# Optimization experiments

Measured on AMD Instinct MI355X. Metric: run time of the kernel, lower is better.

The kernel has to match this reference:

```python
import jax, jax.numpy as jnp
import numpy as np

NUM_USERS = 100000
NUM_MOVIES = 50000
NUM_EDGES = 4000000
USER_FEAT = 24
MOVIE_FEAT = 404
HID = 64
GENRES = 3


def setup_inputs() -> dict:
    key = jax.random.key(0)
    ks = jax.random.split(key, 16)
    inp = {
        'x_user': jax.random.normal(ks[0], (NUM_USERS, USER_FEAT), jnp.float32),
        'x_movie': jax.random.normal(ks[1], (NUM_MOVIES, MOVIE_FEAT), jnp.float32),
        'edge_src': jax.random.randint(ks[2], (NUM_EDGES,), 0, NUM_USERS, jnp.int32),
        'edge_dst': jax.random.randint(ks[3], (NUM_EDGES,), 0, NUM_MOVIES, jnp.int32),
        'W_user': jax.random.normal(ks[4], (HID, USER_FEAT), jnp.float32) * 0.1,
        'b_user': jax.random.normal(ks[5], (HID,), jnp.float32) * 0.1,
        'W_movie': jax.random.normal(ks[6], (HID, MOVIE_FEAT), jnp.float32) * 0.05,
        'b_movie': jax.random.normal(ks[7], (HID,), jnp.float32) * 0.1,
        'Wl1_um': jax.random.normal(ks[8], (HID, HID), jnp.float32) * 0.1,
        'bl1_um': jax.random.normal(ks[9], (HID,), jnp.float32) * 0.1,
        'Wr1_um': jax.random.normal(ks[10], (HID, HID), jnp.float32) * 0.1,
        'Wl1_mu': jax.random.normal(ks[11], (HID, HID), jnp.float32) * 0.1,
        'bl1_mu': jax.random.normal(ks[12], (HID,), jnp.float32) * 0.1,
        'Wr1_mu': jax.random.normal(ks[13], (HID, HID), jnp.float32) * 0.1,
        'Wl2_um': jax.random.normal(ks[14], (GENRES, HID), jnp.float32) * 0.1,
        'bl2_um': jnp.zeros((GENRES,), jnp.float32),
        'Wr2_um': jax.random.normal(ks[15], (GENRES, HID), jnp.float32) * 0.1,
    }
    return inp


def _mean_agg(src_x, src_idx, dst_idx, num_dst):
    # gather messages [E, C], scatter-sum to dst, divide by degree (mean aggr)
    msg = src_x[src_idx]
    s = jax.ops.segment_sum(msg, dst_idx, num_segments=num_dst)
    cnt = jax.ops.segment_sum(jnp.ones_like(dst_idx, jnp.float32), dst_idx, num_segments=num_dst)
    return s / jnp.maximum(cnt, 1.0)[:, None]


def _sage(agg, x_dst, Wl, bl, Wr):
    # SAGEConv: lin_l(mean_aggr(x_j)) + lin_r(x_dst); bias only on lin_l
    return agg @ Wl.T + bl + x_dst @ Wr.T


def reference(x_user, x_movie, edge_src, edge_dst, W_user, b_user, W_movie, b_movie,
              Wl1_um, bl1_um, Wr1_um, Wl1_mu, bl1_mu, Wr1_mu, Wl2_um, bl2_um, Wr2_um):
    nu, nm = x_user.shape[0], x_movie.shape[0]
    # input projections
    hu = x_user @ W_user.T + b_user    # [U, H]
    hm = x_movie @ W_movie.T + b_movie  # [M, H]
    # layer 1 (hetero: one SAGEConv per edge type; undirected -> both directions)
    m1 = _sage(_mean_agg(hu, edge_src, edge_dst, nm), hm, Wl1_um, bl1_um, Wr1_um)
    u1 = _sage(_mean_agg(hm, edge_dst, edge_src, nu), hu, Wl1_mu, bl1_mu, Wr1_mu)
    m1 = jax.nn.relu(m1)
    u1 = jax.nn.relu(u1)
    # dropout is identity in eval mode
    # layer 2: only movie output is returned
    out = _sage(_mean_agg(u1, edge_src, edge_dst, nm), m1, Wl2_um, bl2_um, Wr2_um)
    return out
```

## Files before the change

kernel.cpp:

```cpp
#include <hip/hip_runtime.h>


constexpr int NU = 100000;
constexpr int NM = 50000;
constexpr int NE = 4000000;
constexpr int FU = 24;
constexpr int FM = 404;
constexpr int HD = 64;

constexpr int BSH = 8;
constexpr int MBK = (NM + 255) >> BSH;
constexpr int UBK = (NU + 255) >> BSH;
constexpr int NBK = MBK + UBK;
constexpr int EPB = 8192;
constexpr int CAPE = 28672;

static inline size_t alignup(size_t x) { return (x + 255) & ~size_t(255); }

__device__ __forceinline__ float bf2f(unsigned short h) {
  return __uint_as_float(((unsigned int)h) << 16);
}
__device__ __forceinline__ unsigned short f2bf(float f) {
  unsigned int u = __float_as_uint(f);
  u = (u + 0x7FFFu + ((u >> 16) & 1u)) >> 16;
  return (unsigned short)u;
}
__device__ __forceinline__ float2 unpk(unsigned u) {
  return make_float2(__uint_as_float(u << 16), __uint_as_float(u & 0xFFFF0000u));
}
__device__ __forceinline__ float fp8dec(unsigned v) {
  unsigned u = ((v & 0x80u) << 24) | ((v & 0x7Fu) << 20);
  return __uint_as_float(u) * 0x1p120f;
}
__device__ __forceinline__ unsigned char f2fp8(float f) {
  float a = fminf(fabsf(f), 448.0f);
  unsigned u = __float_as_uint(a * 0x1p-120f);
  u = u + 0x7FFFFu + ((u >> 20) & 1u);
  return (unsigned char)(((u >> 20) & 0x7Fu) | ((__float_as_uint(f) >> 24) & 0x80u));
}

typedef __attribute__((ext_vector_type(2))) float f2v;

#if __has_builtin(__builtin_amdgcn_cvt_pk_f32_fp8)
#define FP8_HW 1
#endif

__device__ __forceinline__ f2v fp8lo(unsigned w) {
#ifdef FP8_HW
  return __builtin_amdgcn_cvt_pk_f32_fp8(w, false);
#else
  f2v r; r.x = fp8dec(w); r.y = fp8dec(w >> 8); return r;
#endif
}
__device__ __forceinline__ f2v fp8hi(unsigned w) {
#ifdef FP8_HW
  return __builtin_amdgcn_cvt_pk_f32_fp8(w, true);
#else
  f2v r; r.x = fp8dec(w >> 16); r.y = fp8dec(w >> 24); return r;
#endif
}

using bf16x8 = __attribute__((ext_vector_type(8))) short;
using f32x4  = __attribute__((ext_vector_type(4))) float;


__global__ __launch_bounds__(256) void histB_kernel(const int* __restrict__ src,
                                                    const int* __restrict__ dst,
                                                    int* __restrict__ bh) {
  __shared__ int h[NBK];
  for (int i = threadIdx.x; i < NBK; i += 256) h[i] = 0;
  __syncthreads();
  int idx = blockIdx.x * 256 + threadIdx.x;
  int stride = gridDim.x * 256;
  for (int i = idx; i < NE; i += stride) {
    atomicAdd(&h[dst[i] >> BSH], 1);
    atomicAdd(&h[MBK + (src[i] >> BSH)], 1);
  }
  __syncthreads();
  for (int i = threadIdx.x; i < NBK; i += 256) {
    int c = h[i];
    if (c) atomicAdd(&bh[i], c);
  }
}

__global__ __launch_bounds__(1024) void scanB_kernel(const int* __restrict__ bh,
                                                     int* __restrict__ bbase_m,
                                                     int* __restrict__ bbase_u,
                                                     int* __restrict__ bcur_m,
                                                     int* __restrict__ bcur_u) {
  __shared__ int tmp[1024];
  int t = threadIdx.x;
  int vm = (t < MBK) ? bh[t] : 0;
  tmp[t] = vm;
  __syncthreads();
  for (int off = 1; off < 1024; off <<= 1) {
    int v = (t >= off) ? tmp[t - off] : 0;
    __syncthreads();
    tmp[t] += v;
    __syncthreads();
  }
  if (t < MBK) {
    int e = tmp[t] - vm;
    bbase_m[t] = e; bcur_m[t] = e;
    if (t == MBK - 1) bbase_m[MBK] = tmp[t];
  }
  __syncthreads();
  int vu = (t < UBK) ? bh[MBK + t] : 0;
  tmp[t] = vu;
  __syncthreads();
  for (int off = 1; off < 1024; off <<= 1) {
    int v = (t >= off) ? tmp[t - off] : 0;
    __syncthreads();
    tmp[t] += v;
    __syncthreads();
  }
  if (t < UBK) {
    int e = tmp[t] - vu;
    bbase_u[t] = e; bcur_u[t] = e;
    if (t == UBK - 1) bbase_u[UBK] = tmp[t];
  }
}

__global__ __launch_bounds__(1024) void passA_kernel(
    const int* __restrict__ src, const int* __restrict__ dst,
    int* __restrict__ bcur_m, int* __restrict__ bcur_u,
    unsigned* __restrict__ stage_m, unsigned* __restrict__ stage_u) {
  __shared__ int hB[NBK];
  __shared__ int cntB[NBK];
  __shared__ int gB[NBK];
  __shared__ int tmp[1024];
  __shared__ unsigned binM[EPB];
  __shared__ unsigned binU[EPB];
  int t = threadIdx.x;
  for (int i = t; i < NBK; i += 1024) hB[i] = 0;
  __syncthreads();
  int e0 = blockIdx.x * EPB + t;
  int sv[8], dv[8], rm[8], ru[8];
#pragma unroll
  for (int k = 0; k < 8; ++k) {
    int e = e0 + k * 1024;
    if (e < NE) {
      int s = src[e], d = dst[e];
      sv[k] = s; dv[k] = d;
      rm[k] = atomicAdd(&hB[d >> BSH], 1);
      ru[k] = atomicAdd(&hB[MBK + (s >> BSH)], 1);
    } else {
      sv[k] = -1;
    }
  }
  __syncthreads();
  int cm = (t < MBK) ? hB[t] : 0;
  tmp[t] = cm;
  __syncthreads();
  for (int off = 1; off < 1024; off <<= 1) {
    int v = (t >= off) ? tmp[t - off] : 0;
    __syncthreads();
    tmp[t] += v;
    __syncthreads();
  }
  int lofsM = tmp[t] - cm;
  __syncthreads();
  int cu_ = (t < UBK) ? hB[MBK + t] : 0;
  tmp[t] = cu_;
  __syncthreads();
  for (int off = 1; off < 1024; off <<= 1) {
    int v = (t >= off) ? tmp[t - off] : 0;
    __syncthreads();
    tmp[t] += v;
    __syncthreads();
  }
  int lofsU = tmp[t] - cu_;
  __syncthreads();
  if (t < MBK) { cntB[t] = cm; hB[t] = lofsM; }
  if (t < UBK) { cntB[MBK + t] = cu_; hB[MBK + t] = lofsU; }
  __syncthreads();
#pragma unroll
  for (int k = 0; k < 8; ++k) {
    if (sv[k] >= 0) {
      int s = sv[k], d = dv[k];
      binM[hB[d >> BSH] + rm[k]] = ((unsigned)(d & 255) << 24) | (unsigned)s;
      binU[hB[MBK + (s >> BSH)] + ru[k]] = ((unsigned)(s & 255) << 24) | (unsigned)d;
    }
  }
  __syncthreads();
  for (int b = t; b < NBK; b += 1024) {
    int cc = cntB[b];
    if (cc) {
      int gb = (b < MBK) ? atomicAdd(&bcur_m[b], cc) : atomicAdd(&bcur_u[b - MBK], cc);
      gB[b] = gb - hB[b];
    }
  }
  __syncthreads();
  int wv = t >> 6, ln = t & 63;
  for (int b = wv; b < MBK; b += 16) {
    int cc = cntB[b], lo = hB[b], go = hB[b] + gB[b];
    for (int j = ln; j < cc; j += 64) stage_m[go + j] = binM[lo + j];
  }
  for (int b = wv; b < UBK; b += 16) {
    int cc = cntB[MBK + b], lo = hB[MBK + b], go = hB[MBK + b] + gB[MBK + b];
    for (int j = ln; j < cc; j += 64) stage_u[go + j] = binU[lo + j];
  }
}

__global__ __launch_bounds__(1024) void passB_kernel(
    const int* __restrict__ bbase_m, const int* __restrict__ bbase_u,
    const unsigned* __restrict__ stage_m, const unsigned* __restrict__ stage_u,
    int* __restrict__ csr_m, int* __restrict__ csr_u,
    int* __restrict__ rp_m, int* __restrict__ rp_u) {
  __shared__ int cnt[256];
  __shared__ int sc[256];
  extern __shared__ unsigned sbuf[];
  int b = blockIdx.x;
  const unsigned* stage; int* csr; int* rp; int idbase, ntot, bb, be;
  if (b < MBK) {
    stage = stage_m; csr = csr_m; rp = rp_m;
    idbase = b << BSH; ntot = NM;
    bb = bbase_m[b]; be = bbase_m[b + 1];
  } else {
    int c = b - MBK;
    stage = stage_u; csr = csr_u; rp = rp_u;
    idbase = c << BSH; ntot = NU;
    bb = bbase_u[c]; be = bbase_u[c + 1];
  }
  int nloc = min(256, ntot - idbase);
  int t = threadIdx.x;
  int span = be - bb;
  if (t < 256) cnt[t] = 0;
  __syncthreads();
  for (int j = bb + t; j < be; j += 1024) atomicAdd(&cnt[stage[j] >> 24], 1);
  __syncthreads();
  int c0 = (t < 256) ? cnt[t] : 0;
  if (t < 256) sc[t] = c0;
  __syncthreads();
  for (int off = 1; off < 256; off <<= 1) {
    int v = 0;
    if (t < 256 && t >= off) v = sc[t - off];
    __syncthreads();
    if (t < 256) sc[t] += v;
    __syncthreads();
  }
  if (t < nloc) {
    rp[idbase + t] = bb + sc[t] - c0;
    cnt[t] = sc[t] - c0;
  }
  if (t == 0 && idbase + nloc == ntot) rp[ntot] = be;
  __syncthreads();
  if (span <= CAPE) {
    for (int j = bb + t; j < be; j += 1024) {
      unsigned e = stage[j];
      int pos = atomicAdd(&cnt[e >> 24], 1);
      sbuf[pos] = e & 0xFFFFFFu;
    }
    __syncthreads();
    for (int j = t; j < span; j += 1024) csr[bb + j] = (int)sbuf[j];
  } else {
    for (int j = bb + t; j < be; j += 1024) {
      unsigned e = stage[j];
      int pos = atomicAdd(&cnt[e >> 24], 1);
      csr[bb + pos] = (int)(e & 0xFFFFFFu);
    }
  }
}


__global__ void convXu_kernel(const float* __restrict__ xu, unsigned char* __restrict__ xu8) {
  int i = blockIdx.x * 256 + threadIdx.x;
  if (i < NU * 32) {
    int r = i >> 5, c = i & 31;
    xu8[i] = (c < FU) ? f2fp8(xu[r * FU + c]) : 0;
  }
}

__global__ void convXu16_kernel(const float* __restrict__ xu, unsigned short* __restrict__ xb) {
  int i = blockIdx.x * 256 + threadIdx.x;
  if (i < NU * 32) {
    int r = i >> 5, c = i & 31;
    unsigned short v = 0;
    if (c < FU) v = f2bf(xu[r * FU + c]);
    else if (c == 31) v = 0x3F80;
    xb[i] = v;
  }
}

__global__ void convW_kernel(const float* __restrict__ W, unsigned short* __restrict__ Wb,
                             int n) {
  int i = blockIdx.x * 256 + threadIdx.x;
  if (i < n) Wb[i] = f2bf(W[i]);
}

__global__ void convWum_kernel(const float* __restrict__ Wl, const float* __restrict__ Wu,
                               const float* __restrict__ bu, const float* __restrict__ Wr,
                               unsigned short* __restrict__ W96) {
  int i = blockIdx.x * 256 + threadIdx.x;
  if (i >= 64 * 96) return;
  int h = i / 96, k = i - h * 96;
  float v = 0.f;
  if (k < FU) {
    for (int j = 0; j < 64; ++j) v += Wl[h * 64 + j] * Wu[j * FU + k];
  } else if (k == 31) {
    for (int j = 0; j < 64; ++j) v += Wl[h * 64 + j] * bu[j];
  } else if (k >= 32) {
    v = Wr[h * 64 + (k - 32)];
  }
  W96[i] = f2bf(v);
}

__global__ void convWmu_kernel(const float* __restrict__ Wl, const float* __restrict__ Wr,
                               const float* __restrict__ Wu, const float* __restrict__ bu,
                               unsigned short* __restrict__ W96) {
  int i = blockIdx.x * 256 + threadIdx.x;
  if (i >= 64 * 96) return;
  int h = i / 96, k = i - h * 96;
  float v = 0.f;
  if (k < 64) {
    v = Wl[h * 64 + k];
  } else if (k < 64 + FU) {
    for (int j = 0; j < 64; ++j) v += Wr[h * 64 + j] * Wu[j * FU + (k - 64)];
  } else if (k == 95) {
    for (int j = 0; j < 64; ++j) v += Wr[h * 64 + j] * bu[j];
  }
  W96[i] = f2bf(v);
}

__global__ __launch_bounds__(256) void proj_movie_kernel(
    const float* __restrict__ xm, const unsigned short* __restrict__ Wb,
    const float* __restrict__ bm, unsigned short* __restrict__ hm,
    unsigned char* __restrict__ hm8) {
  __shared__ unsigned short Xs[64][72];
  __shared__ unsigned short Ws[64][72];
  int t = threadIdx.x;
  int lane = t & 63, wid = t >> 6;
  int row0 = blockIdx.x * 64;
  int r0 = wid * 16;
  f32x4 acc[4];
#pragma unroll
  for (int nt = 0; nt < 4; ++nt) acc[nt] = (f32x4){0.f, 0.f, 0.f, 0.f};

  for (int k0 = 0; k0 < 448; k0 += 64) {
    int kc = min(64, FM - k0);
    __syncthreads();
    for (int i = t; i < 1024; i += 256) {
      int r = i >> 4, c4 = i & 15;
      float4 v = make_float4(0.f, 0.f, 0.f, 0.f);
      if (c4 * 4 < kc && row0 + r < NM)
        v = *(const float4*)(xm + (size_t)(row0 + r) * FM + k0 + c4 * 4);
      ushort4 o;
      o.x = f2bf(v.x); o.y = f2bf(v.y); o.z = f2bf(v.z); o.w = f2bf(v.w);
      *(ushort4*)&Xs[r][c4 * 4] = o;
    }
    for (int i = t; i < 1024; i += 256) {
      int h = i >> 4, c4 = i & 15;
      uint2 v = make_uint2(0u, 0u);
      if (c4 * 4 < kc)
        v = *(const uint2*)(Wb + (size_t)h * FM + k0 + c4 * 4);
      *(uint2*)&Ws[h][c4 * 4] = v;
    }
    __syncthreads();
#pragma unroll
    for (int kk = 0; kk < 64; kk += 32) {
      bf16x8 a = *(const bf16x8*)&Xs[r0 + (lane & 15)][kk + (lane >> 4) * 8];
#pragma unroll
      for (int nt = 0; nt < 4; ++nt) {
        bf16x8 b = *(const bf16x8*)&Ws[nt * 16 + (lane & 15)][kk + (lane >> 4) * 8];
        acc[nt] = __builtin_amdgcn_mfma_f32_16x16x32_bf16(a, b, acc[nt], 0, 0, 0);
      }
    }
  }
  int col = lane & 15;
  int rbase = r0 + (lane >> 4) * 4;
#pragma unroll
  for (int nt = 0; nt < 4; ++nt) {
    float b = bm[nt * 16 + col];
#pragma unroll
    for (int j = 0; j < 4; ++j) {
      int row = row0 + rbase + j;
      if (row < NM) {
        float v = acc[nt][j] + b;
        hm[(size_t)row * HD + nt * 16 + col] = f2bf(v);
        hm8[(size_t)row * HD + nt * 16 + col] = f2fp8(v);
      }
    }
  }
}


__global__ __launch_bounds__(256) void agg24z_kernel(
    const unsigned char* __restrict__ xu8, const int* __restrict__ rp,
    const int* __restrict__ csr, unsigned short* __restrict__ a24,
    float* __restrict__ zagg, int n) {
  int wid = threadIdx.x >> 6, lane = threadIdx.x & 63;
  int row = blockIdx.x * 4 + wid;
  if (row >= n) return;
  int beg = rp[row], end = rp[row + 1];
  int g = lane >> 2;
  int fq = lane & 3;
  const unsigned char* tb = xu8 + fq * 8;
  f2v a01 = {0.f, 0.f}, a23 = {0.f, 0.f}, a45 = {0.f, 0.f}, a67 = {0.f, 0.f};
  int i = beg;
  for (; i + 32 <= end; i += 32) {
    unsigned o0 = (unsigned)csr[i + g] << 5;
    unsigned o1 = (unsigned)csr[i + 16 + g] << 5;
    uint2 w0 = *(const uint2*)(tb + o0);
    uint2 w1 = *(const uint2*)(tb + o1);
    a01 += fp8lo(w0.x) + fp8lo(w1.x);
    a23 += fp8hi(w0.x) + fp8hi(w1.x);
    a45 += fp8lo(w0.y) + fp8lo(w1.y);
    a67 += fp8hi(w0.y) + fp8hi(w1.y);
  }
  for (; i < end; i += 16) {
    int idx = i + g;
    if (idx < end) {
      unsigned o = (unsigned)csr[idx] << 5;
      uint2 w = *(const uint2*)(tb + o);
      a01 += fp8lo(w.x); a23 += fp8hi(w.x);
      a45 += fp8lo(w.y); a67 += fp8hi(w.y);
    }
  }
  float a[8] = {a01.x, a01.y, a23.x, a23.y, a45.x, a45.y, a67.x, a67.y};
#pragma unroll
  for (int off = 4; off < 64; off <<= 1)
#pragma unroll
    for (int j = 0; j < 8; ++j) a[j] += __shfl_xor(a[j], off);
  if (g == 0) {
    float inv = 1.0f / fmaxf((float)(end - beg), 1.0f);
    uint4 o;
    o.x = (unsigned)f2bf(a[0] * inv) | ((unsigned)f2bf(a[1] * inv) << 16);
    o.y = (unsigned)f2bf(a[2] * inv) | ((unsigned)f2bf(a[3] * inv) << 16);
    o.z = (unsigned)f2bf(a[4] * inv) | ((unsigned)f2bf(a[5] * inv) << 16);
    o.w = (unsigned)f2bf(a[6] * inv) | ((unsigned)f2bf(a[7] * inv) << 16);
    if (fq == 3) {
      o.w = (o.w & 0xFFFFu) | ((end > beg ? 0x3F80u : 0u) << 16);
      *(float4*)(zagg + (size_t)row * 4) =
          make_float4(a[0] * inv, a[1] * inv, a[2] * inv, 0.f);
    }
    *(uint4*)(a24 + (size_t)row * 32 + fq * 8) = o;
  }
}


__global__ __launch_bounds__(256) void aggU_kernel(
    const unsigned char* __restrict__ tab8, const int* __restrict__ rp,
    const int* __restrict__ csr, unsigned short* __restrict__ out, int n) {
  int wid = threadIdx.x >> 6, lane = threadIdx.x & 63;
  int row = blockIdx.x * 4 + wid;
  if (row >= n) return;
  int beg = rp[row], end = rp[row + 1];
  int g = lane >> 3;
  int fq = lane & 7;
  const unsigned char* tb = tab8 + fq * 8;
  f2v a01 = {0.f, 0.f}, a23 = {0.f, 0.f}, a45 = {0.f, 0.f}, a67 = {0.f, 0.f};
  int i = beg;
  for (; i + 32 <= end; i += 32) {
    unsigned o0 = (unsigned)csr[i + g] << 6;
    unsigned o1 = (unsigned)csr[i + 8 + g] << 6;
    unsigned o2 = (unsigned)csr[i + 16 + g] << 6;
    unsigned o3 = (unsigned)csr[i + 24 + g] << 6;
    uint2 w0 = *(const uint2*)(tb + o0);
    uint2 w1 = *(const uint2*)(tb + o1);
    uint2 w2 = *(const uint2*)(tb + o2);
    uint2 w3 = *(const uint2*)(tb + o3);
    a01 += (fp8lo(w0.x) + fp8lo(w1.x)) + (fp8lo(w2.x) + fp8lo(w3.x));
    a23 += (fp8hi(w0.x) + fp8hi(w1.x)) + (fp8hi(w2.x) + fp8hi(w3.x));
    a45 += (fp8lo(w0.y) + fp8lo(w1.y)) + (fp8lo(w2.y) + fp8lo(w3.y));
    a67 += (fp8hi(w0.y) + fp8hi(w1.y)) + (fp8hi(w2.y) + fp8hi(w3.y));
  }
  for (; i + 16 <= end; i += 16) {
    unsigned o0 = (unsigned)csr[i + g] << 6;
    unsigned o1 = (unsigned)csr[i + 8 + g] << 6;
    uint2 w0 = *(const uint2*)(tb + o0);
    uint2 w1 = *(const uint2*)(tb + o1);
    a01 += fp8lo(w0.x) + fp8lo(w1.x);
    a23 += fp8hi(w0.x) + fp8hi(w1.x);
    a45 += fp8lo(w0.y) + fp8lo(w1.y);
    a67 += fp8hi(w0.y) + fp8hi(w1.y);
  }
  for (; i < end; i += 8) {
    int idx = i + g;
    if (idx < end) {
      unsigned o = (unsigned)csr[idx] << 6;
      uint2 w = *(const uint2*)(tb + o);
      a01 += fp8lo(w.x); a23 += fp8hi(w.x);
      a45 += fp8lo(w.y); a67 += fp8hi(w.y);
    }
  }
  float a[8] = {a01.x, a01.y, a23.x, a23.y, a45.x, a45.y, a67.x, a67.y};
#pragma unroll
  for (int off = 8; off < 64; off <<= 1)
#pragma unroll
    for (int j = 0; j < 8; ++j) a[j] += __shfl_xor(a[j], off);
  if (g == 0) {
    float inv = 1.0f / fmaxf((float)(end - beg), 1.0f);
    uint4 o;
    o.x = (unsigned)f2bf(a[0] * inv) | ((unsigned)f2bf(a[1] * inv) << 16);
    o.y = (unsigned)f2bf(a[2] * inv) | ((unsigned)f2bf(a[3] * inv) << 16);
    o.z = (unsigned)f2bf(a[4] * inv) | ((unsigned)f2bf(a[5] * inv) << 16);
    o.w = (unsigned)f2bf(a[6] * inv) | ((unsigned)f2bf(a[7] * inv) << 16);
    *(uint4*)(out + (size_t)row * HD + fq * 8) = o;
  }
}


__global__ __launch_bounds__(256) void sage_um_kernel(
    const unsigned short* __restrict__ a24, const unsigned short* __restrict__ hm,
    const unsigned short* __restrict__ W96, const float* __restrict__ bl,
    unsigned short* __restrict__ m1, int n) {
  __shared__ unsigned short Xs[64][104];
  __shared__ unsigned short Ws[64][104];
  int t = threadIdx.x;
  int lane = t & 63, wid = t >> 6;
  int row0 = blockIdx.x * 64;
  int r0 = wid * 16;
  for (int i = t; i < 768; i += 256) {
    int h = i / 12, g = i - h * 12;
    *(uint4*)&Ws[h][g * 8] = *(const uint4*)(W96 + (size_t)h * 96 + g * 8);
  }
  for (int i = t; i < 768; i += 256) {
    int r = i / 12, g = i - r * 12;
    uint4 v = make_uint4(0u, 0u, 0u, 0u);
    if (row0 + r < n) {
      if (g < 4) v = *(const uint4*)(a24 + (size_t)(row0 + r) * 32 + g * 8);
      else       v = *(const uint4*)(hm + (size_t)(row0 + r) * HD + (g - 4) * 8);
    }
    *(uint4*)&Xs[r][g * 8] = v;
  }
  __syncthreads();
  f32x4 acc[4];
#pragma unroll
  for (int nt = 0; nt < 4; ++nt) acc[nt] = (f32x4){0.f, 0.f, 0.f, 0.f};
#pragma unroll
  for (int kk = 0; kk < 96; kk += 32) {
    bf16x8 a = *(const bf16x8*)&Xs[r0 + (lane & 15)][kk + (lane >> 4) * 8];
#pragma unroll
    for (int nt = 0; nt < 4; ++nt) {
      bf16x8 b = *(const bf16x8*)&Ws[nt * 16 + (lane & 15)][kk + (lane >> 4) * 8];
      acc[nt] = __builtin_amdgcn_mfma_f32_16x16x32_bf16(a, b, acc[nt], 0, 0, 0);
    }
  }
  int col = lane & 15;
  int rbase = r0 + (lane >> 4) * 4;
#pragma unroll
  for (int nt = 0; nt < 4; ++nt) {
    float b = bl[nt * 16 + col];
#pragma unroll
    for (int j = 0; j < 4; ++j) {
      int row = row0 + rbase + j;
      if (row < n)
        m1[(size_t)row * HD + nt * 16 + col] = f2bf(fmaxf(acc[nt][j] + b, 0.f));
    }
  }
}


__global__ __launch_bounds__(256) void sage96u_kernel(
    const unsigned short* __restrict__ agg, const unsigned short* __restrict__ xb,
    const unsigned short* __restrict__ W96, const float* __restrict__ bl,
    unsigned short* __restrict__ u1, int n) {
  __shared__ unsigned short Xs[64][104];
  __shared__ unsigned short Ws[64][104];
  int t = threadIdx.x;
  int lane = t & 63, wid = t >> 6;
  int row0 = blockIdx.x * 64;
  int r0 = wid * 16;
  for (int i = t; i < 768; i += 256) {
    int h = i / 12, g = i - h * 12;
    *(uint4*)&Ws[h][g * 8] = *(const uint4*)(W96 + (size_t)h * 96 + g * 8);
  }
  for (int i = t; i < 768; i += 256) {
    int r = i / 12, g = i - r * 12;
    uint4 v = make_uint4(0u, 0u, 0u, 0u);
    if (row0 + r < n) {
      if (g < 8) v = *(const uint4*)(agg + (size_t)(row0 + r) * HD + g * 8);
      else       v = *(const uint4*)(xb + (size_t)(row0 + r) * 32 + (g - 8) * 8);
    }
    *(uint4*)&Xs[r][g * 8] = v;
  }
  __syncthreads();
  f32x4 acc[4];
#pragma unroll
  for (int nt = 0; nt < 4; ++nt) acc[nt] = (f32x4){0.f, 0.f, 0.f, 0.f};
#pragma unroll
  for (int kk = 0; kk < 96; kk += 32) {
    bf16x8 a = *(const bf16x8*)&Xs[r0 + (lane & 15)][kk + (lane >> 4) * 8];
#pragma unroll
    for (int nt = 0; nt < 4; ++nt) {
      bf16x8 b = *(const bf16x8*)&Ws[nt * 16 + (lane & 15)][kk + (lane >> 4) * 8];
      acc[nt] = __builtin_amdgcn_mfma_f32_16x16x32_bf16(a, b, acc[nt], 0, 0, 0);
    }
  }
  int col = lane & 15;
  int rbase = r0 + (lane >> 4) * 4;
#pragma unroll
  for (int nt = 0; nt < 4; ++nt) {
    float b = bl[nt * 16 + col];
#pragma unroll
    for (int j = 0; j < 4; ++j) {
      int row = row0 + rbase + j;
      if (row < n)
        u1[(size_t)row * HD + nt * 16 + col] = f2bf(fmaxf(acc[nt][j] + b, 0.f));
    }
  }
}


__global__ __launch_bounds__(256) void zproj_kernel(
    const unsigned short* __restrict__ u1, const float* __restrict__ Wl2,
    unsigned char* __restrict__ xu8) {
  __shared__ float W[3][64];
  int t = threadIdx.x;
  if (t < 192) W[t / 64][t & 63] = Wl2[t];
  __syncthreads();
  int wid = t >> 6, lane = t & 63;
  int g = lane >> 4, fq = lane & 15;
  int row = blockIdx.x * 16 + wid * 4 + g;
  if (row >= NU) return;
  uint2 v = *(const uint2*)(u1 + (size_t)row * HD + fq * 4);
  float2 p0 = unpk(v.x), p1 = unpk(v.y);
  int f = fq * 4;
  float z0 = p0.x * W[0][f] + p0.y * W[0][f + 1] + p1.x * W[0][f + 2] + p1.y * W[0][f + 3];
  float z1 = p0.x * W[1][f] + p0.y * W[1][f + 1] + p1.x * W[1][f + 2] + p1.y * W[1][f + 3];
  float z2 = p0.x * W[2][f] + p0.y * W[2][f + 1] + p1.x * W[2][f + 2] + p1.y * W[2][f + 3];
#pragma unroll
  for (int off = 1; off < 16; off <<= 1) {
    z0 += __shfl_xor(z0, off);
    z1 += __shfl_xor(z1, off);
    z2 += __shfl_xor(z2, off);
  }
  if (fq == 0) {
    unsigned w = (unsigned)f2fp8(z0) | ((unsigned)f2fp8(z1) << 8)
               | ((unsigned)f2fp8(z2) << 16);
    *(unsigned*)(xu8 + (size_t)row * 32 + 24) = w;
  }
}

__global__ void out2_kernel(const float* __restrict__ zagg,
                            const unsigned short* __restrict__ m1,
                            const float* __restrict__ Wr2, const float* __restrict__ bl2,
                            float* __restrict__ out, int n) {
  int wid = threadIdx.x >> 6, lane = threadIdx.x & 63;
  int row = blockIdx.x * 4 + wid;
  if (row >= n) return;
  float mm = bf2f(m1[(size_t)row * HD + lane]);
#pragma unroll
  for (int g = 0; g < 3; ++g) {
    float p = mm * Wr2[g * HD + lane];
#pragma unroll
    for (int off = 32; off > 0; off >>= 1) p += __shfl_down(p, off);
    if (lane == 0) out[row * 3 + g] = p + zagg[row * 4 + g] + bl2[g];
  }
}


extern "C" void kernel_launch(void* const* d_in, const int* in_sizes, int n_in,
                              void* d_out, int out_size, void* d_ws, size_t ws_size,
                              hipStream_t stream) {
  const float* x_user  = (const float*)d_in[0];
  const float* x_movie = (const float*)d_in[1];
  const int*   e_src   = (const int*)d_in[2];
  const int*   e_dst   = (const int*)d_in[3];
  const float* W_user  = (const float*)d_in[4];
  const float* b_user  = (const float*)d_in[5];
  const float* W_movie = (const float*)d_in[6];
  const float* b_movie = (const float*)d_in[7];
  const float* Wl1_um  = (const float*)d_in[8];
  const float* bl1_um  = (const float*)d_in[9];
  const float* Wr1_um  = (const float*)d_in[10];
  const float* Wl1_mu  = (const float*)d_in[11];
  const float* bl1_mu  = (const float*)d_in[12];
  const float* Wr1_mu  = (const float*)d_in[13];
  const float* Wl2_um  = (const float*)d_in[14];
  const float* bl2_um  = (const float*)d_in[15];
  const float* Wr2_um  = (const float*)d_in[16];
  float* outp = (float*)d_out;

  char* p = (char*)d_ws;
  size_t off = 0;
  auto take = [&](size_t bytes) { void* r = p + off; off += alignup(bytes); return r; };

  int* rp_m    = (int*)take(size_t(NM + 1) * 4);
  int* rp_u    = (int*)take(size_t(NU + 1) * 4);
  int* bh      = (int*)take(size_t(NBK) * 4);
  int* bbase_m = (int*)take(size_t(MBK + 1) * 4);
  int* bbase_u = (int*)take(size_t(UBK + 1) * 4);
  int* bcur_m  = (int*)take(size_t(MBK) * 4);
  int* bcur_u  = (int*)take(size_t(UBK) * 4);
  int* csr_m   = (int*)take(size_t(NE) * 4);
  int* csr_u   = (int*)take(size_t(NE) * 4);

  size_t ov_base = off;
  unsigned* stage_m = (unsigned*)take(size_t(NE) * 4);
  unsigned* stage_u = (unsigned*)take(size_t(NE) * 4);
  size_t stage_end = off;
  off = ov_base;
  unsigned short* hm    = (unsigned short*)take(size_t(NM) * HD * 2);
  unsigned short* u1    = (unsigned short*)take(size_t(NU) * HD * 2);
  unsigned short* m1    = (unsigned short*)take(size_t(NM) * HD * 2);
  unsigned short* aggb  = (unsigned short*)take(size_t(NU) * HD * 2);
  unsigned char*  xu8   = (unsigned char*)take(size_t(NU) * 32);
  unsigned char*  hm8   = (unsigned char*)take(size_t(NM) * HD);
  unsigned short* a24   = (unsigned short*)take(size_t(NM) * 32 * 2);
  unsigned short* xub16 = (unsigned short*)take(size_t(NU) * 32 * 2);
  if (off < stage_end) off = stage_end;
  float* zagg = (float*)take(size_t(NM) * 16);
  unsigned short* Wb    = (unsigned short*)take(size_t(HD) * FM * 2);
  unsigned short* Wum96 = (unsigned short*)take(size_t(HD) * 96 * 2);
  unsigned short* Wmu96 = (unsigned short*)take(size_t(HD) * 96 * 2);
  if (off > ws_size) return;

  const int TB = 256;

  hipMemsetAsync(bh, 0, size_t(NBK) * 4, stream);
  histB_kernel<<<512, 256, 0, stream>>>(e_src, e_dst, bh);
  scanB_kernel<<<1, 1024, 0, stream>>>(bh, bbase_m, bbase_u, bcur_m, bcur_u);
  passA_kernel<<<(NE + EPB - 1) / EPB, 1024, 0, stream>>>(e_src, e_dst, bcur_m, bcur_u,
                                                          stage_m, stage_u);
  passB_kernel<<<NBK, 1024, CAPE * 4, stream>>>(bbase_m, bbase_u, stage_m, stage_u,
                                                csr_m, csr_u, rp_m, rp_u);

  convW_kernel<<<(HD * FM + 255) / 256, 256, 0, stream>>>(W_movie, Wb, HD * FM);
  convWum_kernel<<<(64 * 96 + 255) / 256, 256, 0, stream>>>(Wl1_um, W_user, b_user,
                                                            Wr1_um, Wum96);
  convWmu_kernel<<<(64 * 96 + 255) / 256, 256, 0, stream>>>(Wl1_mu, Wr1_mu, W_user,
                                                            b_user, Wmu96);
  convXu_kernel<<<(NU * 32 + 255) / 256, 256, 0, stream>>>(x_user, xu8);
  convXu16_kernel<<<(NU * 32 + 255) / 256, 256, 0, stream>>>(x_user, xub16);
  proj_movie_kernel<<<(NM + 63) / 64, TB, 0, stream>>>(x_movie, Wb, b_movie, hm, hm8);

  aggU_kernel<<<(NU + 3) / 4, TB, 0, stream>>>(hm8, rp_u, csr_u, aggb, NU);
  sage96u_kernel<<<(NU + 63) / 64, TB, 0, stream>>>(aggb, xub16, Wmu96, bl1_mu, u1, NU);
  zproj_kernel<<<(NU + 15) / 16, TB, 0, stream>>>(u1, Wl2_um, xu8);

  agg24z_kernel<<<(NM + 3) / 4, TB, 0, stream>>>(xu8, rp_m, csr_m, a24, zagg, NM);
  sage_um_kernel<<<(NM + 63) / 64, TB, 0, stream>>>(a24, hm, Wum96, bl1_um, m1, NM);

  out2_kernel<<<(NM + 3) / 4, TB, 0, stream>>>(zagg, m1, Wr2_um, bl2_um, outp, NM);
}
```

Baseline: 274.7 us.

## Map one row per 8-lane group in gather-aggregation kernels, dropping shuffle reductions

Both CSR mean-aggregation kernels now assign each row to an 8-lane group instead of a whole wavefront. Each lane walks all of that row's edges serially, unrolled by 4, and owns a fixed feature slice. This removes the cross-lane shuffle reduction and the idle lanes on short rows, and lets 8 rows share a wave with full-width output stores. In exchange each lane does a sequential edge walk with more dependent loads per row, and rows of uneven degree within one wave cause divergence.

```diff
diff --git a/kernel.cpp b/kernel.cpp
--- a/kernel.cpp
+++ b/kernel.cpp
@@ -58,6 +58,9 @@
 #else
   f2v r; r.x = fp8dec(w >> 16); r.y = fp8dec(w >> 24); return r;
 #endif
+}
+__device__ __forceinline__ unsigned pk2bf(float x, float y) {
+  return (unsigned)f2bf(x) | ((unsigned)f2bf(y) << 16);
 }
 
 using bf16x8 = __attribute__((ext_vector_type(8))) short;
@@ -389,52 +392,40 @@
     const int* __restrict__ csr, unsigned short* __restrict__ a24,
     float* __restrict__ zagg, int n) {
   int wid = threadIdx.x >> 6, lane = threadIdx.x & 63;
-  int row = blockIdx.x * 4 + wid;
+  int g = lane >> 3, fq = lane & 7;
+  int row = blockIdx.x * 32 + wid * 8 + g;
   if (row >= n) return;
   int beg = rp[row], end = rp[row + 1];
-  int g = lane >> 2;
-  int fq = lane & 3;
-  const unsigned char* tb = xu8 + fq * 8;
-  f2v a01 = {0.f, 0.f}, a23 = {0.f, 0.f}, a45 = {0.f, 0.f}, a67 = {0.f, 0.f};
+  const unsigned char* tb = xu8 + fq * 4;
+  f2v a01 = {0.f, 0.f}, a23 = {0.f, 0.f};
   int i = beg;
-  for (; i + 32 <= end; i += 32) {
-    unsigned o0 = (unsigned)csr[i + g] << 5;
-    unsigned o1 = (unsigned)csr[i + 16 + g] << 5;
-    uint2 w0 = *(const uint2*)(tb + o0);
-    uint2 w1 = *(const uint2*)(tb + o1);
-    a01 += fp8lo(w0.x) + fp8lo(w1.x);
-    a23 += fp8hi(w0.x) + fp8hi(w1.x);
-    a45 += fp8lo(w0.y) + fp8lo(w1.y);
-    a67 += fp8hi(w0.y) + fp8hi(w1.y);
-  }
-  for (; i < end; i += 16) {
-    int idx = i + g;
-    if (idx < end) {
-      unsigned o = (unsigned)csr[idx] << 5;
-      uint2 w = *(const uint2*)(tb + o);
-      a01 += fp8lo(w.x); a23 += fp8hi(w.x);
-      a45 += fp8lo(w.y); a67 += fp8hi(w.y);
-    }
-  }
-  float a[8] = {a01.x, a01.y, a23.x, a23.y, a45.x, a45.y, a67.x, a67.y};
-#pragma unroll
-  for (int off = 4; off < 64; off <<= 1)
-#pragma unroll
-    for (int j = 0; j < 8; ++j) a[j] += __shfl_xor(a[j], off);
-  if (g == 0) {
-    float inv = 1.0f / fmaxf((float)(end - beg), 1.0f);
-    uint4 o;
-    o.x = (unsigned)f2bf(a[0] * inv) | ((unsigned)f2bf(a[1] * inv) << 16);
-    o.y = (unsigned)f2bf(a[2] * inv) | ((unsigned)f2bf(a[3] * inv) << 16);
-    o.z = (unsigned)f2bf(a[4] * inv) | ((unsigned)f2bf(a[5] * inv) << 16);
-    o.w = (unsigned)f2bf(a[6] * inv) | ((unsigned)f2bf(a[7] * inv) << 16);
-    if (fq == 3) {
-      o.w = (o.w & 0xFFFFu) | ((end > beg ? 0x3F80u : 0u) << 16);
-      *(float4*)(zagg + (size_t)row * 4) =
-          make_float4(a[0] * inv, a[1] * inv, a[2] * inv, 0.f);
-    }
-    *(uint4*)(a24 + (size_t)row * 32 + fq * 8) = o;
-  }
+  for (; i + 4 <= end; i += 4) {
+    unsigned o0 = (unsigned)csr[i] << 5;
+    unsigned o1 = (unsigned)csr[i + 1] << 5;
+    unsigned o2 = (unsigned)csr[i + 2] << 5;
+    unsigned o3 = (unsigned)csr[i + 3] << 5;
+    unsigned w0 = *(const unsigned*)(tb + o0);
+    unsigned w1 = *(const unsigned*)(tb + o1);
+    unsigned w2 = *(const unsigned*)(tb + o2);
+    unsigned w3 = *(const unsigned*)(tb + o3);
+    a01 += (fp8lo(w0) + fp8lo(w1)) + (fp8lo(w2) + fp8lo(w3));
+    a23 += (fp8hi(w0) + fp8hi(w1)) + (fp8hi(w2) + fp8hi(w3));
+  }
+  for (; i < end; ++i) {
+    unsigned w = *(const unsigned*)(tb + ((unsigned)csr[i] << 5));
+    a01 += fp8lo(w);
+    a23 += fp8hi(w);
+  }
+  float inv = 1.0f / fmaxf((float)(end - beg), 1.0f);
+  uint2 o;
+  o.x = pk2bf(a01.x * inv, a01.y * inv);
+  o.y = pk2bf(a23.x * inv, a23.y * inv);
+  if (fq == 7)
+    o.y = (o.y & 0xFFFFu) | ((end > beg ? 0x3F80u : 0u) << 16);
+  if (fq == 6)
+    *(float4*)(zagg + (size_t)row * 4) =
+        make_float4(a01.x * inv, a01.y * inv, a23.x * inv, 0.f);
+  *(uint2*)(a24 + (size_t)row * 32 + fq * 4) = o;
 }
 
 
@@ -442,19 +433,18 @@
     const unsigned char* __restrict__ tab8, const int* __restrict__ rp,
     const int* __restrict__ csr, unsigned short* __restrict__ out, int n) {
   int wid = threadIdx.x >> 6, lane = threadIdx.x & 63;
-  int row = blockIdx.x * 4 + wid;
+  int g = lane >> 3, fq = lane & 7;
+  int row = blockIdx.x * 32 + wid * 8 + g;
   if (row >= n) return;
   int beg = rp[row], end = rp[row + 1];
-  int g = lane >> 3;
-  int fq = lane & 7;
   const unsigned char* tb = tab8 + fq * 8;
   f2v a01 = {0.f, 0.f}, a23 = {0.f, 0.f}, a45 = {0.f, 0.f}, a67 = {0.f, 0.f};
   int i = beg;
-  for (; i + 32 <= end; i += 32) {
-    unsigned o0 = (unsigned)csr[i + g] << 6;
-    unsigned o1 = (unsigned)csr[i + 8 + g] << 6;
-    unsigned o2 = (unsigned)csr[i + 16 + g] << 6;
-    unsigned o3 = (unsigned)csr[i + 24 + g] << 6;
+  for (; i + 4 <= end; i += 4) {
+    unsigned o0 = (unsigned)csr[i] << 6;
+    unsigned o1 = (unsigned)csr[i + 1] << 6;
+    unsigned o2 = (unsigned)csr[i + 2] << 6;
+    unsigned o3 = (unsigned)csr[i + 3] << 6;
     uint2 w0 = *(const uint2*)(tb + o0);
     uint2 w1 = *(const uint2*)(tb + o1);
     uint2 w2 = *(const uint2*)(tb + o2);
@@ -464,39 +454,18 @@
     a45 += (fp8lo(w0.y) + fp8lo(w1.y)) + (fp8lo(w2.y) + fp8lo(w3.y));
     a67 += (fp8hi(w0.y) + fp8hi(w1.y)) + (fp8hi(w2.y) + fp8hi(w3.y));
   }
-  for (; i + 16 <= end; i += 16) {
-    unsigned o0 = (unsigned)csr[i + g] << 6;
-    unsigned o1 = (unsigned)csr[i + 8 + g] << 6;
-    uint2 w0 = *(const uint2*)(tb + o0);
-    uint2 w1 = *(const uint2*)(tb + o1);
-    a01 += fp8lo(w0.x) + fp8lo(w1.x);
-    a23 += fp8hi(w0.x) + fp8hi(w1.x);
-    a45 += fp8lo(w0.y) + fp8lo(w1.y);
-    a67 += fp8hi(w0.y) + fp8hi(w1.y);
-  }
-  for (; i < end; i += 8) {
-    int idx = i + g;
-    if (idx < end) {
-      unsigned o = (unsigned)csr[idx] << 6;
-      uint2 w = *(const uint2*)(tb + o);
-      a01 += fp8lo(w.x); a23 += fp8hi(w.x);
-      a45 += fp8lo(w.y); a67 += fp8hi(w.y);
-    }
-  }
-  float a[8] = {a01.x, a01.y, a23.x, a23.y, a45.x, a45.y, a67.x, a67.y};
-#pragma unroll
-  for (int off = 8; off < 64; off <<= 1)
-#pragma unroll
-    for (int j = 0; j < 8; ++j) a[j] += __shfl_xor(a[j], off);
-  if (g == 0) {
-    float inv = 1.0f / fmaxf((float)(end - beg), 1.0f);
-    uint4 o;
-    o.x = (unsigned)f2bf(a[0] * inv) | ((unsigned)f2bf(a[1] * inv) << 16);
-    o.y = (unsigned)f2bf(a[2] * inv) | ((unsigned)f2bf(a[3] * inv) << 16);
-    o.z = (unsigned)f2bf(a[4] * inv) | ((unsigned)f2bf(a[5] * inv) << 16);
-    o.w = (unsigned)f2bf(a[6] * inv) | ((unsigned)f2bf(a[7] * inv) << 16);
-    *(uint4*)(out + (size_t)row * HD + fq * 8) = o;
-  }
+  for (; i < end; ++i) {
+    uint2 w = *(const uint2*)(tb + ((unsigned)csr[i] << 6));
+    a01 += fp8lo(w.x); a23 += fp8hi(w.x);
+    a45 += fp8lo(w.y); a67 += fp8hi(w.y);
+  }
+  float inv = 1.0f / fmaxf((float)(end - beg), 1.0f);
+  uint4 o;
+  o.x = pk2bf(a01.x * inv, a01.y * inv);
+  o.y = pk2bf(a23.x * inv, a23.y * inv);
+  o.z = pk2bf(a45.x * inv, a45.y * inv);
+  o.w = pk2bf(a67.x * inv, a67.y * inv);
+  *(uint4*)(out + (size_t)row * HD + fq * 8) = o;
 }
 
 
@@ -725,11 +694,11 @@
   convXu16_kernel<<<(NU * 32 + 255) / 256, 256, 0, stream>>>(x_user, xub16);
   proj_movie_kernel<<<(NM + 63) / 64, TB, 0, stream>>>(x_movie, Wb, b_movie, hm, hm8);
 
-  aggU_kernel<<<(NU + 3) / 4, TB, 0, stream>>>(hm8, rp_u, csr_u, aggb, NU);
+  aggU_kernel<<<(NU + 31) / 32, TB, 0, stream>>>(hm8, rp_u, csr_u, aggb, NU);
   sage96u_kernel<<<(NU + 63) / 64, TB, 0, stream>>>(aggb, xub16, Wmu96, bl1_mu, u1, NU);
   zproj_kernel<<<(NU + 15) / 16, TB, 0, stream>>>(u1, Wl2_um, xu8);
 
-  agg24z_kernel<<<(NM + 3) / 4, TB, 0, stream>>>(xu8, rp_m, csr_m, a24, zagg, NM);
+  agg24z_kernel<<<(NM + 31) / 32, TB, 0, stream>>>(xu8, rp_m, csr_m, a24, zagg, NM);
   sage_um_kernel<<<(NM + 63) / 64, TB, 0, stream>>>(a24, hm, Wum96, bl1_um, m1, NM);
 
   out2_kernel<<<(NM + 3) / 4, TB, 0, stream>>>(zagg, m1, Wr2_um, bl2_um, outp, NM);
```

Measured after the change: 270.1 us. About the same (-1.7%).
